# Kernel optimization log

Measured on AMD Instinct MI355X. Metric: run time of the kernel, lower is better.

Reference implementation:

```python
import jax, jax.numpy as jnp
import numpy as np

N = 10000      # nodes
E = 160000     # edges (before self-loops)
H = 4          # heads
C = 256        # per-head channels
D_IN = 512
D_OUT = 512
NEG_SLOPE = 0.2  # PyG GATConv default negative_slope


def gat_conv(x, src, dst, W, a_src, a_dst, bias):
    """PyG-style GATConv with concat=True. x:[n,d_in], W:[d_in,H*C]."""
    n = x.shape[0]
    h = (x @ W).reshape(n, H, C)                       # [n,H,C]
    al_s = jnp.einsum('nhc,hc->nh', h, a_src)          # [n,H]
    al_d = jnp.einsum('nhc,hc->nh', h, a_dst)          # [n,H]
    e = jax.nn.leaky_relu(al_s[src] + al_d[dst], NEG_SLOPE)   # [Etot,H]
    # segment softmax over edges grouped by destination node
    emax = jax.ops.segment_max(e, dst, num_segments=n)
    w = jnp.exp(e - emax[dst])
    denom = jax.ops.segment_sum(w, dst, num_segments=n)
    alpha = w / denom[dst]                             # [Etot,H]
    out = jax.ops.segment_sum(h[src] * alpha[:, :, None], dst, num_segments=n)
    return out.reshape(n, H * C) + bias


def setup_inputs() -> dict:
    key = jax.random.key(0)
    ks = jax.random.split(key, 13)
    s = 0.05
    return {
        'x': jax.random.normal(ks[0], (N, D_IN), jnp.float32),
        'edge_index': jax.random.randint(ks[1], (2, E), 0, N, dtype=jnp.int32),
        'W1': jax.random.normal(ks[2], (D_IN, H * C), jnp.float32) * s,
        'a_src1': jax.random.normal(ks[3], (H, C), jnp.float32) * s,
        'a_dst1': jax.random.normal(ks[4], (H, C), jnp.float32) * s,
        'b1': jnp.zeros((H * C,), jnp.float32),
        'W2': jax.random.normal(ks[5], (H * C, H * C), jnp.float32) * s,
        'a_src2': jax.random.normal(ks[6], (H, C), jnp.float32) * s,
        'a_dst2': jax.random.normal(ks[7], (H, C), jnp.float32) * s,
        'b2': jnp.zeros((H * C,), jnp.float32),
        'Wfc': jax.random.normal(ks[8], (H * C, D_OUT), jnp.float32) * s,
        'bfc': jnp.zeros((D_OUT,), jnp.float32),
    }


def reference(x, edge_index, W1, a_src1, a_dst1, b1, W2, a_src2, a_dst2, b2, Wfc, bfc):
    # PyG GATConv default add_self_loops=True
    loop = jnp.arange(N, dtype=edge_index.dtype)
    src = jnp.concatenate([edge_index[0], loop])
    dst = jnp.concatenate([edge_index[1], loop])
    h = jax.nn.relu(gat_conv(x, src, dst, W1, a_src1, a_dst1, b1))
    # dropout is identity in eval mode
    h = jax.nn.relu(gat_conv(h, src, dst, W2, a_src2, a_dst2, b2))
    return h @ Wfc + bfc
```

## Files before the change

### kernel.cpp

```cpp
#include <hip/hip_runtime.h>

#define NND 10000
#define NED 160000
#define NET 170000
#define MP  10112
#define DH  1024
#define DIN 512
#define DOUT 512
#define SCB 40

#define NB_CONV 5056
#define NB_T1   512
#define NB_T2   1024
#define NB_T3   512
#define NB_Z    80
#define NB_AP1  512
#define NB_AP2  1024
#define NB_PREP (NB_CONV + NB_T1 + NB_T2 + NB_T3 + NB_Z + NB_AP1 + NB_AP2)

#define NB_CNT  665
#define NB_ALV1 2500

typedef unsigned short u16;
typedef __attribute__((ext_vector_type(8))) short short8_t;
typedef __attribute__((ext_vector_type(4))) float f32x4_t;

__device__ __forceinline__ u16 f2bf(float f) {
  unsigned u = __float_as_uint(f);
  return (u16)((u + 0x7fffu + ((u >> 16) & 1u)) >> 16);
}
__device__ __forceinline__ float bf2f(u16 b) {
  return __uint_as_float(((unsigned)b) << 16);
}
__device__ __forceinline__ float bflo(unsigned u) { return __uint_as_float(u << 16); }
__device__ __forceinline__ float bfhi(unsigned u) { return __uint_as_float(u & 0xffff0000u); }
__device__ __forceinline__ float lrelu(float v) { return v > 0.f ? v : 0.2f * v; }

__device__ __forceinline__ void gl_lds16(const void* g, void* l) {
  __builtin_amdgcn_global_load_lds(
      (const __attribute__((address_space(1))) unsigned int*)g,
      (__attribute__((address_space(3))) unsigned int*)l, 16, 0, 0);
}


__device__ __forceinline__ void dev_transpose(const float* __restrict__ W,
                                              u16* __restrict__ WT,
                                              int K, int Nt, int bx, int by, int t) {
  __shared__ float s[32][33];
  const int kt = by * 32, nt = bx * 32;
  const int tx = t & 31, ty = t >> 5;
#pragma unroll
  for (int i = 0; i < 32; i += 8)
    s[ty + i][tx] = W[(size_t)(kt + ty + i) * Nt + nt + tx];
  __syncthreads();
#pragma unroll
  for (int i = 0; i < 32; i += 8)
    WT[(size_t)(nt + ty + i) * K + kt + tx] = f2bf(s[tx][ty + i]);
}

__device__ __forceinline__ void dev_aproj(const float* __restrict__ W,
                                          const float* __restrict__ a_s,
                                          const float* __restrict__ a_d,
                                          float* __restrict__ pv, int K,
                                          int p, int ln) {
  const int h = p & 3, k = p >> 2;
  const float4 wv  = *(const float4*)(W + (size_t)k * DH + h * 256 + ln * 4);
  const float4 asv = *(const float4*)(a_s + h * 256 + ln * 4);
  const float4 adv = *(const float4*)(a_d + h * 256 + ln * 4);
  float ps = wv.x * asv.x + wv.y * asv.y + wv.z * asv.z + wv.w * asv.w;
  float pd = wv.x * adv.x + wv.y * adv.y + wv.z * adv.z + wv.w * adv.w;
#pragma unroll
  for (int off = 32; off; off >>= 1) {
    ps += __shfl_xor(ps, off);
    pd += __shfl_xor(pd, off);
  }
  if (ln == 0) {
    pv[(h * 2 + 0) * K + k] = ps;
    pv[(h * 2 + 1) * K + k] = pd;
  }
}

template <int K>
__device__ __forceinline__ void dev_alv(const u16* __restrict__ rows,
                                        const float* __restrict__ pv,
                                        float* __restrict__ als,
                                        float* __restrict__ ald,
                                        int n, int ln) {
  constexpr int EPL = K / 64;
  float xr[EPL];
  const uint4* rp4 = (const uint4*)(rows + (size_t)n * K + ln * EPL);
#pragma unroll
  for (int q = 0; q < EPL / 8; q++) {
    uint4 hv = rp4[q];
    xr[q * 8 + 0] = bflo(hv.x); xr[q * 8 + 1] = bfhi(hv.x);
    xr[q * 8 + 2] = bflo(hv.y); xr[q * 8 + 3] = bfhi(hv.y);
    xr[q * 8 + 4] = bflo(hv.z); xr[q * 8 + 5] = bfhi(hv.z);
    xr[q * 8 + 6] = bflo(hv.w); xr[q * 8 + 7] = bfhi(hv.w);
  }
  float d[8];
#pragma unroll
  for (int v = 0; v < 8; v++) {
    const float* pvv = pv + v * K + ln * EPL;
    float s = 0.f;
#pragma unroll
    for (int j = 0; j < EPL; j++) s += xr[j] * pvv[j];
#pragma unroll
    for (int off = 32; off; off >>= 1) s += __shfl_xor(s, off);
    d[v] = s;
  }
  if (ln == 0) {
    als[n * 4 + 0] = d[0]; ald[n * 4 + 0] = d[1];
    als[n * 4 + 1] = d[2]; ald[n * 4 + 1] = d[3];
    als[n * 4 + 2] = d[4]; ald[n * 4 + 2] = d[5];
    als[n * 4 + 3] = d[6]; ald[n * 4 + 3] = d[7];
  }
}


__global__ void k_prep(const float* __restrict__ x, u16* __restrict__ xb,
                       const float* __restrict__ W1, u16* __restrict__ w1t,
                       const float* __restrict__ W2, u16* __restrict__ w2t,
                       const float* __restrict__ Wfc, u16* __restrict__ wft,
                       int* __restrict__ indeg,
                       u16* __restrict__ hbp, u16* __restrict__ h2bp,
                       const float* __restrict__ as1, const float* __restrict__ ad1,
                       const float* __restrict__ as2, const float* __restrict__ ad2,
                       float* __restrict__ pv1, float* __restrict__ pv2) {
  int b = blockIdx.x, t = threadIdx.x;
  if (b < NB_CONV) {
    int i = b * 256 + t;
    float4 v = make_float4(0.f, 0.f, 0.f, 0.f);
    if (i < NND * DIN / 4) v = ((const float4*)x)[i];
    ushort4 o;
    o.x = f2bf(v.x); o.y = f2bf(v.y); o.z = f2bf(v.z); o.w = f2bf(v.w);
    ((ushort4*)xb)[i] = o;
    return;
  }
  b -= NB_CONV;
  if (b < NB_T1) { dev_transpose(W1, w1t, DIN, DH, b & 31, b >> 5, t); return; }
  b -= NB_T1;
  if (b < NB_T2) { dev_transpose(W2, w2t, DH, DH, b & 31, b >> 5, t); return; }
  b -= NB_T2;
  if (b < NB_T3) { dev_transpose(Wfc, wft, DH, DOUT, b & 15, b >> 4, t); return; }
  b -= NB_T3;
  if (b < NB_Z) {
    int i = b * 256 + t;
    const uint4 z = make_uint4(0, 0, 0, 0);
    if (i < (MP - NND) * DH / 8) { ((uint4*)hbp)[i] = z; ((uint4*)h2bp)[i] = z; }
    if (i < NND) indeg[i] = 0;
    return;
  }
  b -= NB_Z;
  if (b < NB_AP1) { dev_aproj(W1, as1, ad1, pv1, DIN, b * 4 + (t >> 6), t & 63); return; }
  b -= NB_AP1;
  { dev_aproj(W2, as2, ad2, pv2, DH, b * 4 + (t >> 6), t & 63); }
}


__global__ void k_cnt_alv(const int* __restrict__ ei, int* __restrict__ indeg,
                          const u16* __restrict__ xb, const float* __restrict__ pv1,
                          float* __restrict__ als1, float* __restrict__ ald1) {
  const int b = blockIdx.x, t = threadIdx.x;
  if (b < NB_CNT) {
    int e = b * 256 + t;
    if (e < NET) {
      int dst = (e < NED) ? ei[NED + e] : (e - NED);
      atomicAdd(&indeg[dst], 1);
    }
    return;
  }
  const int n = (b - NB_CNT) * 4 + (t >> 6);
  if (n < NND) dev_alv<DIN>(xb, pv1, als1, ald1, n, t & 63);
}

__global__ __launch_bounds__(64) void k_alv2(const u16* __restrict__ rows,
                                             const float* __restrict__ pv,
                                             float* __restrict__ als,
                                             float* __restrict__ ald) {
  dev_alv<DH>(rows, pv, als, ald, blockIdx.x, threadIdx.x);
}


__global__ void k_scan1(const int* __restrict__ indeg, int* __restrict__ rowp,
                        int* __restrict__ bsum) {
  __shared__ int ws[4];
  const int b = blockIdx.x, t = threadIdx.x, wv = t >> 6, ln = t & 63;
  const int i = b * 256 + t;
  int v = (i < NND) ? indeg[i] : 0;
  int sc = v;
#pragma unroll
  for (int off = 1; off < 64; off <<= 1) {
    int xx = __shfl_up(sc, off);
    if (ln >= off) sc += xx;
  }
  if (ln == 63) ws[wv] = sc;
  __syncthreads();
  if (t == 0) {
    int a = 0;
#pragma unroll
    for (int k = 0; k < 4; k++) { int tmp = ws[k]; ws[k] = a; a += tmp; }
    bsum[b] = a;
  }
  __syncthreads();
  sc += ws[wv];
  if (i < NND) rowp[i + 1] = sc;
}

__global__ void k_scan2(int* __restrict__ bsum) {
  int t = threadIdx.x;
  int v = (t < SCB) ? bsum[t] : 0;
  int sc = v;
#pragma unroll
  for (int off = 1; off < 64; off <<= 1) {
    int xx = __shfl_up(sc, off);
    if (t >= off) sc += xx;
  }
  if (t < SCB) bsum[t] = sc - v;
}

__global__ void k_scan3(int* __restrict__ rowp, const int* __restrict__ bsum,
                        int* __restrict__ cursor) {
  const int b = blockIdx.x, t = threadIdx.x;
  const int i = b * 256 + t;
  if (i < NND) { rowp[i + 1] += bsum[b]; cursor[i] = 0; }
  if (i == 0) rowp[0] = 0;
}

__global__ void k_fill(const int* __restrict__ ei, const int* __restrict__ rowp,
                       int* __restrict__ cursor, int* __restrict__ colsrc) {
  int e = blockIdx.x * 256 + threadIdx.x;
  if (e >= NET) return;
  int src, dst;
  if (e < NED) { src = ei[e]; dst = ei[NED + e]; }
  else         { src = dst = e - NED; }
  int pos = rowp[dst] + atomicAdd(&cursor[dst], 1);
  colsrc[pos] = src;
}


template <int KD, int GX, bool HAS_BIAS, bool GUARD, bool OUTBF>
__global__ __launch_bounds__(256) void k_gemm(const u16* __restrict__ A,
                                              const u16* __restrict__ BT,
                                              float* __restrict__ Cf,
                                              u16* __restrict__ Cb,
                                              const float* __restrict__ bias,
                                              int ldc, int mvalid) {
  __shared__ __align__(16) u16 As[128 * 32];
  __shared__ __align__(16) u16 Bs[128 * 32];
  const int tid = threadIdx.x;
  const int lane = tid & 63;
  const int w = tid >> 6;
  const int wr = w >> 1, wc = w & 1;
  const int l15 = lane & 15;
  const int kg = (lane >> 4) * 8;
  const int kgs = kg ^ (((l15 >> 1) & 3) * 8);

  const int nwg = GX * gridDim.y;
  const int bid = blockIdx.y * GX + blockIdx.x;
  const int q = nwg >> 3, r = nwg & 7;
  const int xcd = bid & 7, idx = bid >> 3;
  const int swz = (xcd < r ? xcd * (q + 1) : r * (q + 1) + (xcd - r) * q) + idx;
  const int mt = swz / GX, nt = swz % GX;

  const int flat0 = tid * 8;
  const int row0 = tid >> 2;
  const int kk0 = (((tid & 3) ^ ((tid >> 3) & 3)) * 8);
  const int row1 = 64 + row0;

  const u16* Ab = A + (size_t)(mt * 128) * KD;
  const u16* Bb = BT + (size_t)(nt * 128) * KD;
  const u16* ga0 = Ab + row0 * KD + kk0;
  const u16* ga1 = Ab + row1 * KD + kk0;
  const u16* gb0 = Bb + row0 * KD + kk0;
  const u16* gb1 = Bb + row1 * KD + kk0;
  u16* lA0 = As + flat0;
  u16* lA1 = As + 2048 + flat0;
  u16* lB0 = Bs + flat0;
  u16* lB1 = Bs + 2048 + flat0;

  f32x4_t acc[4][4];
#pragma unroll
  for (int i = 0; i < 4; i++)
#pragma unroll
    for (int j = 0; j < 4; j++)
#pragma unroll
      for (int q2 = 0; q2 < 4; q2++) acc[i][j][q2] = 0.f;

  for (int kt = 0; kt < KD; kt += 32) {
    __syncthreads();
    gl_lds16(ga0 + kt, lA0);
    gl_lds16(ga1 + kt, lA1);
    gl_lds16(gb0 + kt, lB0);
    gl_lds16(gb1 + kt, lB1);
    __syncthreads();
    short8_t af[4], bfr[4];
#pragma unroll
    for (int i = 0; i < 4; i++)
      af[i] = *(const short8_t*)(As + (wr * 64 + i * 16 + l15) * 32 + kgs);
#pragma unroll
    for (int i = 0; i < 4; i++)
      bfr[i] = *(const short8_t*)(Bs + (wc * 64 + i * 16 + l15) * 32 + kgs);
#pragma unroll
    for (int i = 0; i < 4; i++)
#pragma unroll
      for (int j = 0; j < 4; j++)
        acc[i][j] = __builtin_amdgcn_mfma_f32_16x16x32_bf16(af[i], bfr[j], acc[i][j], 0, 0, 0);
  }

  const int rbase = mt * 128 + wr * 64 + (lane >> 4) * 4;
  const int cbase = nt * 128 + wc * 64 + l15;
#pragma unroll
  for (int i = 0; i < 4; i++) {
#pragma unroll
    for (int j = 0; j < 4; j++) {
#pragma unroll
      for (int q2 = 0; q2 < 4; q2++) {
        int rr = rbase + i * 16 + q2;
        int cc = cbase + j * 16;
        if (!GUARD || rr < mvalid) {
          float v = acc[i][j][q2];
          if (HAS_BIAS) v += bias[cc];
          if (OUTBF) Cb[(size_t)rr * ldc + cc] = f2bf(v);
          else       Cf[(size_t)rr * ldc + cc] = v;
        }
      }
    }
  }
}


__global__ __launch_bounds__(64) void k_agg4(const u16* __restrict__ hprojb,
                                             const float* __restrict__ als,
                                             const float* __restrict__ ald,
                                             const int* __restrict__ rowp,
                                             const int* __restrict__ colsrc,
                                             const float* __restrict__ bias,
                                             u16* __restrict__ outb) {
  const int n = blockIdx.x, qh = blockIdx.y, ln = threadIdx.x;
  const int beg = rowp[n], end = rowp[n + 1];
  const float adv = ald[n * 4 + qh];

  float m = -1e30f;
  for (int e = beg + ln; e < end; e += 64)
    m = fmaxf(m, lrelu(als[colsrc[e] * 4 + qh] + adv));
#pragma unroll
  for (int off = 32; off; off >>= 1) m = fmaxf(m, __shfl_xor(m, off));

  const u16* hbase = hprojb + qh * 256 + ln * 4;
  float a0 = 0.f, a1 = 0.f, a2 = 0.f, a3 = 0.f;
  float ds = 0.f;
  int e = beg;
  for (; e + 1 < end; e += 2) {
    int s0 = colsrc[e], s1 = colsrc[e + 1];
    float w0 = __expf(lrelu(als[s0 * 4 + qh] + adv) - m);
    float w1 = __expf(lrelu(als[s1 * 4 + qh] + adv) - m);
    uint2 h0 = *(const uint2*)(hbase + (size_t)s0 * DH);
    uint2 h1 = *(const uint2*)(hbase + (size_t)s1 * DH);
    a0 += bflo(h0.x) * w0; a1 += bfhi(h0.x) * w0;
    a2 += bflo(h0.y) * w0; a3 += bfhi(h0.y) * w0;
    a0 += bflo(h1.x) * w1; a1 += bfhi(h1.x) * w1;
    a2 += bflo(h1.y) * w1; a3 += bfhi(h1.y) * w1;
    ds += w0 + w1;
  }
  if (e < end) {
    int s0 = colsrc[e];
    float w0 = __expf(lrelu(als[s0 * 4 + qh] + adv) - m);
    uint2 h0 = *(const uint2*)(hbase + (size_t)s0 * DH);
    a0 += bflo(h0.x) * w0; a1 += bfhi(h0.x) * w0;
    a2 += bflo(h0.y) * w0; a3 += bfhi(h0.y) * w0;
    ds += w0;
  }

  const float inv = 1.f / ds;
  const float4 bv = *(const float4*)(bias + qh * 256 + ln * 4);
  float o0 = fmaxf(a0 * inv + bv.x, 0.f), o1 = fmaxf(a1 * inv + bv.y, 0.f);
  float o2 = fmaxf(a2 * inv + bv.z, 0.f), o3 = fmaxf(a3 * inv + bv.w, 0.f);
  uint2 ob;
  ob.x = (unsigned)f2bf(o0) | ((unsigned)f2bf(o1) << 16);
  ob.y = (unsigned)f2bf(o2) | ((unsigned)f2bf(o3) << 16);
  *(uint2*)(outb + (size_t)n * DH + qh * 256 + ln * 4) = ob;
}


extern "C" void kernel_launch(void* const* d_in, const int* in_sizes, int n_in,
                              void* d_out, int out_size, void* d_ws, size_t ws_size,
                              hipStream_t stream) {
  const float* x   = (const float*)d_in[0];
  const int*   ei  = (const int*)d_in[1];
  const float* W1  = (const float*)d_in[2];
  const float* as1 = (const float*)d_in[3];
  const float* ad1 = (const float*)d_in[4];
  const float* b1  = (const float*)d_in[5];
  const float* W2  = (const float*)d_in[6];
  const float* as2 = (const float*)d_in[7];
  const float* ad2 = (const float*)d_in[8];
  const float* b2  = (const float*)d_in[9];
  const float* Wfc = (const float*)d_in[10];
  const float* bfc = (const float*)d_in[11];
  float* out = (float*)d_out;
  (void)in_sizes; (void)n_in; (void)out_size; (void)ws_size;

  char* p = (char*)d_ws;
  auto carve = [&](size_t bytes) -> char* {
    char* r = p; p += (bytes + 255) & ~(size_t)255; return r;
  };
  u16*   xb     = (u16*)  carve((size_t)MP * DIN * 2);
  u16*   w1t    = (u16*)  carve((size_t)DH * DIN * 2);
  u16*   w2t    = (u16*)  carve((size_t)DH * DH * 2);
  u16*   wft    = (u16*)  carve((size_t)DOUT * DH * 2);
  u16*   hprojb = (u16*)  carve((size_t)MP * DH * 2);
  u16*   hb     = (u16*)  carve((size_t)MP * DH * 2);
  u16*   h2b    = (u16*)  carve((size_t)MP * DH * 2);
  float* als1   = (float*)carve((size_t)NND * 4 * 4);
  float* ald1   = (float*)carve((size_t)NND * 4 * 4);
  float* als2   = (float*)carve((size_t)NND * 4 * 4);
  float* ald2   = (float*)carve((size_t)NND * 4 * 4);
  float* pv1    = (float*)carve((size_t)8 * DIN * 4);
  float* pv2    = (float*)carve((size_t)8 * DH * 4);
  int*   indeg  = (int*)  carve((size_t)NND * 4);
  int*   rowp   = (int*)  carve((size_t)(NND + 1) * 4);
  int*   cursor = (int*)  carve((size_t)NND * 4);
  int*   colsrc = (int*)  carve((size_t)NET * 4);
  int*   bsum   = (int*)  carve((size_t)SCB * 4);

  k_prep<<<NB_PREP, 256, 0, stream>>>(x, xb, W1, w1t, W2, w2t, Wfc, wft,
      indeg, hb + (size_t)NND * DH, h2b + (size_t)NND * DH,
      as1, ad1, as2, ad2, pv1, pv2);
  k_cnt_alv<<<NB_CNT + NB_ALV1, 256, 0, stream>>>(ei, indeg, xb, pv1, als1, ald1);
  k_scan1<<<SCB, 256, 0, stream>>>(indeg, rowp, bsum);
  k_scan2<<<1, 64, 0, stream>>>(bsum);
  k_scan3<<<SCB, 256, 0, stream>>>(rowp, bsum, cursor);
  k_fill<<<(NET + 255) / 256, 256, 0, stream>>>(ei, rowp, cursor, colsrc);

  k_gemm<DIN, 8, false, false, true><<<dim3(DH / 128, MP / 128), 256, 0, stream>>>(
      xb, w1t, nullptr, hprojb, nullptr, DH, MP);
  k_agg4<<<dim3(NND, 4), 64, 0, stream>>>(hprojb, als1, ald1, rowp, colsrc, b1, hb);

  k_alv2<<<NND, 64, 0, stream>>>(hb, pv2, als2, ald2);
  k_gemm<DH, 8, false, false, true><<<dim3(DH / 128, MP / 128), 256, 0, stream>>>(
      hb, w2t, nullptr, hprojb, nullptr, DH, MP);
  k_agg4<<<dim3(NND, 4), 64, 0, stream>>>(hprojb, als2, ald2, rowp, colsrc, b2, h2b);

  k_gemm<DH, 4, true, true, false><<<dim3(DOUT / 128, MP / 128), 256, 0, stream>>>(
      h2b, wft, out, nullptr, bfc, DOUT, NND);
}
```

Baseline: 227.2 us.

## Fuse layer-2 attention logits into aggregation and drop softmax max pass

The aggregation kernel now processes two heads per 64-lane block, with each lane loading 8 bf16 channels, and unrolls the edge loop by four. The separate max-reduction pass for the segment softmax is removed, so weights are exp(logit) without subtracting the max. The layer-2 attention projections (als2/ald2) are computed in the layer-1 aggregation epilogue via wave reductions and atomicAdd into buffers zeroed in prep. This removes one full edge pass and one kernel launch, but risks exp overflow if the logits grow large, and atomics make the summation order nondeterministic.

After: 210.4 us. -7.4%, faster.

```diff
diff --git a/kernel.cpp b/kernel.cpp
--- a/kernel.cpp
+++ b/kernel.cpp
@@ -125,7 +125,8 @@
                        u16* __restrict__ hbp, u16* __restrict__ h2bp,
                        const float* __restrict__ as1, const float* __restrict__ ad1,
                        const float* __restrict__ as2, const float* __restrict__ ad2,
-                       float* __restrict__ pv1, float* __restrict__ pv2) {
+                       float* __restrict__ pv1, float* __restrict__ pv2,
+                       float* __restrict__ als2, float* __restrict__ ald2) {
   int b = blockIdx.x, t = threadIdx.x;
   if (b < NB_CONV) {
     int i = b * 256 + t;
@@ -147,7 +148,12 @@
     int i = b * 256 + t;
     const uint4 z = make_uint4(0, 0, 0, 0);
     if (i < (MP - NND) * DH / 8) { ((uint4*)hbp)[i] = z; ((uint4*)h2bp)[i] = z; }
-    if (i < NND) indeg[i] = 0;
+    if (i < NND) {
+      indeg[i] = 0;
+      const float4 zf = make_float4(0.f, 0.f, 0.f, 0.f);
+      ((float4*)als2)[i] = zf;
+      ((float4*)ald2)[i] = zf;
+    }
     return;
   }
   b -= NB_Z;
@@ -171,13 +177,6 @@
   }
   const int n = (b - NB_CNT) * 4 + (t >> 6);
   if (n < NND) dev_alv<DIN>(xb, pv1, als1, ald1, n, t & 63);
-}
-
-__global__ __launch_bounds__(64) void k_alv2(const u16* __restrict__ rows,
-                                             const float* __restrict__ pv,
-                                             float* __restrict__ als,
-                                             float* __restrict__ ald) {
-  dev_alv<DH>(rows, pv, als, ald, blockIdx.x, threadIdx.x);
 }
 
 
@@ -329,56 +328,97 @@
 }
 
 
-__global__ __launch_bounds__(64) void k_agg4(const u16* __restrict__ hprojb,
+template <bool FUSE_ALV>
+__global__ __launch_bounds__(64) void k_aggh(const u16* __restrict__ hprojb,
                                              const float* __restrict__ als,
                                              const float* __restrict__ ald,
                                              const int* __restrict__ rowp,
                                              const int* __restrict__ colsrc,
                                              const float* __restrict__ bias,
-                                             u16* __restrict__ outb) {
-  const int n = blockIdx.x, qh = blockIdx.y, ln = threadIdx.x;
+                                             u16* __restrict__ outb,
+                                             const float* __restrict__ pv2,
+                                             float* __restrict__ als2,
+                                             float* __restrict__ ald2) {
+  const int n = blockIdx.x, half = blockIdx.y, ln = threadIdx.x;
   const int beg = rowp[n], end = rowp[n + 1];
-  const float adv = ald[n * 4 + qh];
-
-  float m = -1e30f;
-  for (int e = beg + ln; e < end; e += 64)
-    m = fmaxf(m, lrelu(als[colsrc[e] * 4 + qh] + adv));
-#pragma unroll
-  for (int off = 32; off; off >>= 1) m = fmaxf(m, __shfl_xor(m, off));
-
-  const u16* hbase = hprojb + qh * 256 + ln * 4;
+  const int hsel = 2 * half + (ln >> 5);
+  const float adv = ald[n * 4 + hsel];
+  const u16* hbase = hprojb + half * 512 + ln * 8;
+
   float a0 = 0.f, a1 = 0.f, a2 = 0.f, a3 = 0.f;
+  float a4 = 0.f, a5 = 0.f, a6 = 0.f, a7 = 0.f;
   float ds = 0.f;
   int e = beg;
-  for (; e + 1 < end; e += 2) {
-    int s0 = colsrc[e], s1 = colsrc[e + 1];
-    float w0 = __expf(lrelu(als[s0 * 4 + qh] + adv) - m);
-    float w1 = __expf(lrelu(als[s1 * 4 + qh] + adv) - m);
-    uint2 h0 = *(const uint2*)(hbase + (size_t)s0 * DH);
-    uint2 h1 = *(const uint2*)(hbase + (size_t)s1 * DH);
+  for (; e + 3 < end; e += 4) {
+    int s0 = colsrc[e], s1 = colsrc[e + 1], s2 = colsrc[e + 2], s3 = colsrc[e + 3];
+    float l0 = als[s0 * 4 + hsel], l1 = als[s1 * 4 + hsel];
+    float l2 = als[s2 * 4 + hsel], l3 = als[s3 * 4 + hsel];
+    uint4 h0 = *(const uint4*)(hbase + (size_t)s0 * DH);
+    uint4 h1 = *(const uint4*)(hbase + (size_t)s1 * DH);
+    uint4 h2 = *(const uint4*)(hbase + (size_t)s2 * DH);
+    uint4 h3 = *(const uint4*)(hbase + (size_t)s3 * DH);
+    float w0 = __expf(lrelu(l0 + adv)), w1 = __expf(lrelu(l1 + adv));
+    float w2 = __expf(lrelu(l2 + adv)), w3 = __expf(lrelu(l3 + adv));
     a0 += bflo(h0.x) * w0; a1 += bfhi(h0.x) * w0;
     a2 += bflo(h0.y) * w0; a3 += bfhi(h0.y) * w0;
+    a4 += bflo(h0.z) * w0; a5 += bfhi(h0.z) * w0;
+    a6 += bflo(h0.w) * w0; a7 += bfhi(h0.w) * w0;
     a0 += bflo(h1.x) * w1; a1 += bfhi(h1.x) * w1;
     a2 += bflo(h1.y) * w1; a3 += bfhi(h1.y) * w1;
-    ds += w0 + w1;
-  }
-  if (e < end) {
+    a4 += bflo(h1.z) * w1; a5 += bfhi(h1.z) * w1;
+    a6 += bflo(h1.w) * w1; a7 += bfhi(h1.w) * w1;
+    a0 += bflo(h2.x) * w2; a1 += bfhi(h2.x) * w2;
+    a2 += bflo(h2.y) * w2; a3 += bfhi(h2.y) * w2;
+    a4 += bflo(h2.z) * w2; a5 += bfhi(h2.z) * w2;
+    a6 += bflo(h2.w) * w2; a7 += bfhi(h2.w) * w2;
+    a0 += bflo(h3.x) * w3; a1 += bfhi(h3.x) * w3;
+    a2 += bflo(h3.y) * w3; a3 += bfhi(h3.y) * w3;
+    a4 += bflo(h3.z) * w3; a5 += bfhi(h3.z) * w3;
+    a6 += bflo(h3.w) * w3; a7 += bfhi(h3.w) * w3;
+    ds += (w0 + w1) + (w2 + w3);
+  }
+  for (; e < end; e++) {
     int s0 = colsrc[e];
-    float w0 = __expf(lrelu(als[s0 * 4 + qh] + adv) - m);
-    uint2 h0 = *(const uint2*)(hbase + (size_t)s0 * DH);
+    float w0 = __expf(lrelu(als[s0 * 4 + hsel] + adv));
+    uint4 h0 = *(const uint4*)(hbase + (size_t)s0 * DH);
     a0 += bflo(h0.x) * w0; a1 += bfhi(h0.x) * w0;
     a2 += bflo(h0.y) * w0; a3 += bfhi(h0.y) * w0;
+    a4 += bflo(h0.z) * w0; a5 += bfhi(h0.z) * w0;
+    a6 += bflo(h0.w) * w0; a7 += bfhi(h0.w) * w0;
     ds += w0;
   }
 
   const float inv = 1.f / ds;
-  const float4 bv = *(const float4*)(bias + qh * 256 + ln * 4);
-  float o0 = fmaxf(a0 * inv + bv.x, 0.f), o1 = fmaxf(a1 * inv + bv.y, 0.f);
-  float o2 = fmaxf(a2 * inv + bv.z, 0.f), o3 = fmaxf(a3 * inv + bv.w, 0.f);
-  uint2 ob;
+  const float4 bv0 = *(const float4*)(bias + half * 512 + ln * 8);
+  const float4 bv1 = *(const float4*)(bias + half * 512 + ln * 8 + 4);
+  float o0 = fmaxf(a0 * inv + bv0.x, 0.f), o1 = fmaxf(a1 * inv + bv0.y, 0.f);
+  float o2 = fmaxf(a2 * inv + bv0.z, 0.f), o3 = fmaxf(a3 * inv + bv0.w, 0.f);
+  float o4 = fmaxf(a4 * inv + bv1.x, 0.f), o5 = fmaxf(a5 * inv + bv1.y, 0.f);
+  float o6 = fmaxf(a6 * inv + bv1.z, 0.f), o7 = fmaxf(a7 * inv + bv1.w, 0.f);
+  uint4 ob;
   ob.x = (unsigned)f2bf(o0) | ((unsigned)f2bf(o1) << 16);
   ob.y = (unsigned)f2bf(o2) | ((unsigned)f2bf(o3) << 16);
-  *(uint2*)(outb + (size_t)n * DH + qh * 256 + ln * 4) = ob;
+  ob.z = (unsigned)f2bf(o4) | ((unsigned)f2bf(o5) << 16);
+  ob.w = (unsigned)f2bf(o6) | ((unsigned)f2bf(o7) << 16);
+  *(uint4*)(outb + (size_t)n * DH + half * 512 + ln * 8) = ob;
+
+  if (FUSE_ALV) {
+    const int cb = half * 512 + ln * 8;
+    float ov[8] = {o0, o1, o2, o3, o4, o5, o6, o7};
+#pragma unroll
+    for (int v = 0; v < 8; v++) {
+      const float* pvv = pv2 + (size_t)v * DH + cb;
+      float s = ov[0] * pvv[0] + ov[1] * pvv[1] + ov[2] * pvv[2] + ov[3] * pvv[3] +
+                ov[4] * pvv[4] + ov[5] * pvv[5] + ov[6] * pvv[6] + ov[7] * pvv[7];
+#pragma unroll
+      for (int off = 32; off; off >>= 1) s += __shfl_xor(s, off);
+      if (ln == 0) {
+        int h = v >> 1;
+        if (v & 1) atomicAdd(&ald2[n * 4 + h], s);
+        else       atomicAdd(&als2[n * 4 + h], s);
+      }
+    }
+  }
 }
 
 
@@ -425,7 +465,7 @@
 
   k_prep<<<NB_PREP, 256, 0, stream>>>(x, xb, W1, w1t, W2, w2t, Wfc, wft,
       indeg, hb + (size_t)NND * DH, h2b + (size_t)NND * DH,
-      as1, ad1, as2, ad2, pv1, pv2);
+      as1, ad1, as2, ad2, pv1, pv2, als2, ald2);
   k_cnt_alv<<<NB_CNT + NB_ALV1, 256, 0, stream>>>(ei, indeg, xb, pv1, als1, ald1);
   k_scan1<<<SCB, 256, 0, stream>>>(indeg, rowp, bsum);
   k_scan2<<<1, 64, 0, stream>>>(bsum);
@@ -434,12 +474,13 @@
 
   k_gemm<DIN, 8, false, false, true><<<dim3(DH / 128, MP / 128), 256, 0, stream>>>(
       xb, w1t, nullptr, hprojb, nullptr, DH, MP);
-  k_agg4<<<dim3(NND, 4), 64, 0, stream>>>(hprojb, als1, ald1, rowp, colsrc, b1, hb);
-
-  k_alv2<<<NND, 64, 0, stream>>>(hb, pv2, als2, ald2);
+  k_aggh<true><<<dim3(NND, 2), 64, 0, stream>>>(hprojb, als1, ald1, rowp, colsrc,
+      b1, hb, pv2, als2, ald2);
+
   k_gemm<DH, 8, false, false, true><<<dim3(DH / 128, MP / 128), 256, 0, stream>>>(
       hb, w2t, nullptr, hprojb, nullptr, DH, MP);
-  k_agg4<<<dim3(NND, 4), 64, 0, stream>>>(hprojb, als2, ald2, rowp, colsrc, b2, h2b);
+  k_aggh<false><<<dim3(NND, 2), 64, 0, stream>>>(hprojb, als2, ald2, rowp, colsrc,
+      b2, h2b, nullptr, nullptr, nullptr);
 
   k_gemm<DH, 4, true, true, false><<<dim3(DOUT / 128, MP / 128), 256, 0, stream>>>(
       h2b, wft, out, nullptr, bfc, DOUT, NND);
```
